# Kernel optimization log

Hardware: AMD Instinct MI355X
Metric: run time of the kernel (lower is better)

The kernel has to match this reference:

```python
import jax, jax.numpy as jnp
import numpy as np

B, L, D, H = 4, 2048, 1024, 16
DK = D // H
SCALE = 1.0 / (DK ** 0.5)


def setup_inputs() -> dict:
    key = jax.random.key(0)
    ks = jax.random.split(key, 7)
    std = 1.0 / np.sqrt(D)
    return {
        "q": jax.random.normal(ks[0], (B, L, D), jnp.float32),
        "k": jax.random.normal(ks[1], (B, L, D), jnp.float32),
        "v": jax.random.normal(ks[2], (B, L, D), jnp.float32),
        # torch nn.Linear weights: shape (out_features, in_features)
        "w_q": jax.random.normal(ks[3], (D, D), jnp.float32) * std,
        "w_k": jax.random.normal(ks[4], (D, D), jnp.float32) * std,
        "w_v": jax.random.normal(ks[5], (D, D), jnp.float32) * std,
        "w_o": jax.random.normal(ks[6], (D, D), jnp.float32) * std,
    }


def _split_heads(x):
    # (B, L, D) -> (B, H, L, DK)
    return x.reshape(B, L, H, DK).transpose(0, 2, 1, 3)


def reference(q, k, v, w_q, w_k, w_v, w_o):
    # Linear projections (no bias): y = x @ W^T
    qh = _split_heads(jnp.einsum('bld,ed->ble', q, w_q))
    kh = _split_heads(jnp.einsum('bld,ed->ble', k, w_k))
    vh = _split_heads(jnp.einsum('bld,ed->ble', v, w_v))
    # scaled dot-product attention; score is (B, H, L, L)
    score = jnp.einsum('bhqd,bhkd->bhqk', qh, kh) * SCALE
    probs = jax.nn.softmax(score, axis=-1)  # dropout p=0.0 -> identity
    attn = jnp.einsum('bhqk,bhkd->bhqd', probs, vh)
    # merge heads and output projection
    o = attn.transpose(0, 2, 1, 3).reshape(B, L, D)
    return jnp.einsum('bld,ed->ble', o, w_o)
```

## Files before the change

### kernel.cpp

```cpp
#include <hip/hip_runtime.h>
#include <stdint.h>

typedef unsigned short u16;
typedef __attribute__((ext_vector_type(8))) short short8;
typedef __attribute__((ext_vector_type(4))) float floatx4;

#define DEV __device__ __forceinline__

DEV u16 f2bf(float f) {
  union { float f; unsigned u; } x; x.f = f;
  unsigned u = x.u + 0x7fffu + ((x.u >> 16) & 1u);
  return (u16)(u >> 16);
}
DEV float scrub(float x) {
  return fminf(fmaxf(x, -65504.0f), 65504.0f);
}
DEV void async16(const void* g, void* l) {
  auto gp = reinterpret_cast<const __attribute__((address_space(1))) unsigned int*>(
      reinterpret_cast<uintptr_t>(g));
  auto lp = reinterpret_cast<__attribute__((address_space(3))) unsigned int*>(
      reinterpret_cast<uintptr_t>(l));
  __builtin_amdgcn_global_load_lds(gp, lp, 16, 0, 0);
}
DEV unsigned asu(float f) { union { float f; unsigned u; } x; x.f = f; return x.u; }
DEV float asf(unsigned u) { union { unsigned u; float f; } x; x.u = u; return x.f; }

__global__ void cvt7(const float* __restrict__ a, const float* __restrict__ b,
                     const float* __restrict__ c, const float* __restrict__ w0,
                     const float* __restrict__ w1, const float* __restrict__ w2,
                     const float* __restrict__ w3,
                     u16* __restrict__ oa, u16* __restrict__ ob, u16* __restrict__ oc,
                     u16* __restrict__ o0, u16* __restrict__ o1, u16* __restrict__ o2,
                     u16* __restrict__ o3) {
  constexpr int N4A = 1 << 21;
  constexpr int N4W = 1 << 18;
  int i4 = blockIdx.x * 256 + threadIdx.x;
  const float* s;
  u16* d;
  int off;
  if (i4 < 3 * N4A) {
    int z = i4 >> 21;
    off = i4 & (N4A - 1);
    s = z == 0 ? a : (z == 1 ? b : c);
    d = z == 0 ? oa : (z == 1 ? ob : oc);
  } else {
    int j = i4 - 3 * N4A;
    int z = j >> 18;
    off = j & (N4W - 1);
    s = z == 0 ? w0 : (z == 1 ? w1 : (z == 2 ? w2 : w3));
    d = z == 0 ? o0 : (z == 1 ? o1 : (z == 2 ? o2 : o3));
  }
  float4 v = ((const float4*)s)[off];
  union { u16 h[4]; uint2 u; } o;
  o.h[0] = f2bf(v.x); o.h[1] = f2bf(v.y); o.h[2] = f2bf(v.z); o.h[3] = f2bf(v.w);
  ((uint2*)d)[off] = o.u;
}

__global__ __launch_bounds__(256, 4) void proj3(
    const u16* __restrict__ Xq, const u16* __restrict__ Xk, const u16* __restrict__ Xv,
    const u16* __restrict__ Wq, const u16* __restrict__ Wk, const u16* __restrict__ Wv,
    u16* __restrict__ Oq, u16* __restrict__ Ok, u16* __restrict__ Ov)
{
  constexpr int K = 1024;
  constexpr float SC2 = 0.125f * 1.44269504088896f;
  int flat = blockIdx.x + 8 * (blockIdx.y + 64 * blockIdx.z);
  int swz = (flat & 7) * 192 + (flat >> 3);
  const int bx = swz & 7, by = (swz >> 3) & 63, z = swz >> 9;

  const u16* X = z == 0 ? Xq : (z == 1 ? Xk : Xv);
  const u16* W = z == 0 ? Wq : (z == 1 ? Wk : Wv);
  u16* Out = z == 0 ? Oq : (z == 1 ? Ok : Ov);

  const u16* A = (z < 2) ? W : X;
  const u16* Bp = (z < 2) ? X : W;
  const int m0 = (z < 2) ? bx * 128 : by * 128;
  const int n0 = (z < 2) ? by * 128 : bx * 128;

  const int tid = threadIdx.x;
  const int w = tid >> 6, lane = tid & 63;
  const int quad = lane >> 4, l16 = lane & 15;
  const int wm = (w & 1) * 64, wn = (w >> 1) * 64;

  __shared__ u16 As[128 * 64];
  __shared__ u16 Bs[128 * 64];

  floatx4 acc[4][4];
#pragma unroll
  for (int i = 0; i < 4; ++i)
#pragma unroll
    for (int j = 0; j < 4; ++j) acc[i][j] = (floatx4)0.0f;

  for (int k0 = 0; k0 < K; k0 += 64) {
#pragma unroll
    for (int i = 0; i < 4; ++i) {
      int lin = i * 256 + tid;
      int r = lin >> 3, sp = lin & 7, s = sp ^ (r & 7);
      async16(A + (size_t)(m0 + r) * K + k0 + s * 8, &As[lin * 8]);
    }
#pragma unroll
    for (int i = 0; i < 4; ++i) {
      int lin = i * 256 + tid;
      int r = lin >> 3, sp = lin & 7, s = sp ^ (r & 7);
      async16(Bp + (size_t)(n0 + r) * K + k0 + s * 8, &Bs[lin * 8]);
    }
    asm volatile("s_waitcnt vmcnt(0)" ::: "memory");
    __syncthreads();

#pragma unroll
    for (int kk = 0; kk < 2; ++kk) {
      short8 af[4], bf[4];
#pragma unroll
      for (int mi = 0; mi < 4; ++mi) {
        int r = wm + mi * 16 + l16;
        af[mi] = *(const short8*)&As[r * 64 + (((kk * 4 + quad) ^ (r & 7)) * 8)];
      }
#pragma unroll
      for (int ni = 0; ni < 4; ++ni) {
        int r = wn + ni * 16 + l16;
        bf[ni] = *(const short8*)&Bs[r * 64 + (((kk * 4 + quad) ^ (r & 7)) * 8)];
      }
#pragma unroll
      for (int mi = 0; mi < 4; ++mi)
#pragma unroll
        for (int ni = 0; ni < 4; ++ni)
          acc[mi][ni] = __builtin_amdgcn_mfma_f32_16x16x32_bf16(af[mi], bf[ni], acc[mi][ni], 0, 0, 0);
    }
    __syncthreads();
  }

  const float sc = (z == 0) ? SC2 : 1.0f;
#pragma unroll
  for (int mi = 0; mi < 4; ++mi) {
#pragma unroll
    for (int ni = 0; ni < 4; ++ni) {
      int rr = m0 + wm + mi * 16 + quad * 4;
      int cc = n0 + wn + ni * 16 + l16;
      u16 h0 = f2bf(sc * acc[mi][ni][0]);
      u16 h1 = f2bf(sc * acc[mi][ni][1]);
      u16 h2 = f2bf(sc * acc[mi][ni][2]);
      u16 h3 = f2bf(sc * acc[mi][ni][3]);
      uint2 dw; dw.x = h0 | ((unsigned)h1 << 16); dw.y = h2 | ((unsigned)h3 << 16);
      if (z < 2) {
        int bb = cc >> 11, ll = cc & 2047;
        int hh = rr >> 6, dk0 = rr & 63;
        *(uint2*)&Out[(((size_t)bb * 16 + hh) * 2048 + ll) * 64 + dk0] = dw;
      } else {
        int bb = rr >> 11, ll0 = rr & 2047;
        int hh = cc >> 6, dk = cc & 63;
        *(uint2*)&Out[(((size_t)bb * 16 + hh) * 64 + dk) * 2048 + ll0] = dw;
      }
    }
  }
}

__global__ __launch_bounds__(256, 2) void gemm_out(
    const u16* __restrict__ Ah, const u16* __restrict__ Wo, float* __restrict__ Out)
{
  constexpr int K = 1024;
  const int tid = threadIdx.x;
  const int w = tid >> 6, lane = tid & 63;
  const int quad = lane >> 4, l16 = lane & 15;
  int flat = blockIdx.x + 8 * blockIdx.y;
  int swz = (flat & 7) * 64 + (flat >> 3);
  const int bx = swz & 7, by = swz >> 3;
  const int m0 = by * 128, n0 = bx * 128;
  const int wm = (w & 1) * 64, wn = (w >> 1) * 64;

  __shared__ u16 SM[32768];

  auto stage = [&](int p, int k0) {
#pragma unroll
    for (int i = 0; i < 4; ++i) {
      int lin = i * 256 + tid;
      int r = lin >> 3, sp = lin & 7, s = sp ^ (r & 7);
      int row = m0 + r;
      const u16* ga = Ah + (((size_t)(row >> 11) * 16 + (k0 >> 6)) * 2048 + (row & 2047)) * 64 + s * 8;
      async16(ga, &SM[p * 8192 + lin * 8]);
    }
#pragma unroll
    for (int i = 0; i < 4; ++i) {
      int lin = i * 256 + tid;
      int r = lin >> 3, sp = lin & 7, s = sp ^ (r & 7);
      async16(Wo + (size_t)(n0 + r) * K + k0 + s * 8, &SM[16384 + p * 8192 + lin * 8]);
    }
  };

  floatx4 acc[4][4];
#pragma unroll
  for (int i = 0; i < 4; ++i)
#pragma unroll
    for (int j = 0; j < 4; ++j) acc[i][j] = (floatx4)0.0f;

  stage(0, 0);
  asm volatile("s_waitcnt vmcnt(0)" ::: "memory");
  __syncthreads();

  for (int k0 = 0; k0 < K; k0 += 64) {
    const int p = (k0 >> 6) & 1;
    if (k0 + 64 < K) stage(p ^ 1, k0 + 64);
    const u16* Asp = &SM[p * 8192];
    const u16* Bsp = &SM[16384 + p * 8192];

    __builtin_amdgcn_s_setprio(1);
#pragma unroll
    for (int kk = 0; kk < 2; ++kk) {
      short8 af[4], bf[4];
#pragma unroll
      for (int mi = 0; mi < 4; ++mi) {
        int r = wm + mi * 16 + l16;
        af[mi] = *(const short8*)&Asp[r * 64 + (((kk * 4 + quad) ^ (r & 7)) * 8)];
      }
#pragma unroll
      for (int ni = 0; ni < 4; ++ni) {
        int r = wn + ni * 16 + l16;
        bf[ni] = *(const short8*)&Bsp[r * 64 + (((kk * 4 + quad) ^ (r & 7)) * 8)];
      }
#pragma unroll
      for (int mi = 0; mi < 4; ++mi)
#pragma unroll
        for (int ni = 0; ni < 4; ++ni)
          acc[mi][ni] = __builtin_amdgcn_mfma_f32_16x16x32_bf16(af[mi], bf[ni], acc[mi][ni], 0, 0, 0);
    }
    __builtin_amdgcn_s_setprio(0);

    asm volatile("s_waitcnt vmcnt(0)" ::: "memory");
    __syncthreads();
  }

#pragma unroll
  for (int mi = 0; mi < 4; ++mi)
#pragma unroll
    for (int ni = 0; ni < 4; ++ni) {
      int rr = m0 + wm + mi * 16 + quad * 4;
      int cc = n0 + wn + ni * 16 + l16;
#pragma unroll
      for (int reg = 0; reg < 4; ++reg)
        Out[(size_t)(rr + reg) * 1024 + cc] = scrub(acc[mi][ni][reg]);
    }
}

__global__ __launch_bounds__(256, 4) void attn3(
    const u16* Qh, const u16* __restrict__ Kh,
    const u16* __restrict__ VT, u16* O)
{
  constexpr int L = 2048, DK = 64, H = 16;
  const int tid = threadIdx.x;
  const int w = tid >> 6, lane = tid & 63;
  const int quad = lane >> 4, l16 = lane & 15;
  int flat = blockIdx.x + 16 * (blockIdx.y + 16 * blockIdx.z);
  int swz = (flat & 7) * 128 + (flat >> 3);
  const int q0 = (swz & 15) * 128;
  const int bh = swz >> 4;

  __shared__ u16 SM[4 * 64 * 64];
  u16* const QP = &SM[8192];
  char* const SMb = (char*)&SM[0];

  const u16* Qg = Qh + ((size_t)bh * L + q0) * DK;
  const u16* Kb = Kh + (size_t)bh * L * DK;
  const u16* Vb = VT + (size_t)bh * DK * L;

#pragma unroll
  for (int i = 0; i < 4; ++i) {
    int lin = i * 256 + tid;
    int r = lin >> 3, sp = lin & 7, s = sp ^ (r & 7);
    async16(Qg + (size_t)r * DK + s * 8, &QP[lin * 8]);
  }

  const int rA = tid >> 3;
  const int sA = (tid & 7) ^ (rA & 7);
  const u16* kg0 = Kb + (size_t)rA * DK + sA * 8;
  const u16* kg1 = kg0 + 32 * DK;
  const u16* vg0 = Vb + (size_t)rA * L + sA * 8;
  const u16* vg1 = vg0 + (size_t)32 * L;
  u16* const ldsB0 = &SM[tid * 8];
  u16* const ldsB1 = &SM[8192 + tid * 8];

  async16(kg0, ldsB0);
  async16(kg1, ldsB0 + 2048);
  async16(vg0, ldsB0 + 4096);
  async16(vg1, ldsB0 + 6144);
  kg0 += 64 * DK; kg1 += 64 * DK; vg0 += 64; vg1 += 64;

  asm volatile("s_waitcnt vmcnt(0)" ::: "memory");
  __syncthreads();

  short8 qf[2][2];
#pragma unroll
  for (int mi = 0; mi < 2; ++mi)
#pragma unroll
    for (int kk = 0; kk < 2; ++kk) {
      int r = w * 32 + mi * 16 + l16;
      qf[mi][kk] = *(const short8*)&QP[r * 64 + (((kk * 4 + quad) ^ (r & 7)) * 8)];
    }
  asm volatile("s_waitcnt lgkmcnt(0)" ::: "memory");
  __syncthreads();

  const int l7 = l16 & 7, qh2 = quad >> 1, qo = (quad & 1) * 8;
  int ka[2], vo[4];
#pragma unroll
  for (int kk = 0; kk < 2; ++kk)
    ka[kk] = l16 * 128 + (((kk * 4 + quad) ^ l7) * 16);
#pragma unroll
  for (int j = 0; j < 4; ++j)
    vo[j] = l16 * 128 + (((qh2 + 2 * j) ^ l7) * 16) + qo;

  short8 onesv;
#pragma unroll
  for (int j = 0; j < 8; ++j) onesv[j] = (short)0x3F80;

  floatx4 oT[4][2];
  floatx4 lacc[2];
#pragma unroll
  for (int nd = 0; nd < 4; ++nd)
#pragma unroll
    for (int mi = 0; mi < 2; ++mi) oT[nd][mi] = (floatx4)0.0f;
  lacc[0] = (floatx4)0.0f;
  lacc[1] = (floatx4)0.0f;

  auto body = [&](int PB, u16* ldsN, bool more) {
    if (more) {
      async16(kg0, ldsN);
      async16(kg1, ldsN + 2048);
      async16(vg0, ldsN + 4096);
      async16(vg1, ldsN + 6144);
      kg0 += 64 * DK; kg1 += 64 * DK; vg0 += 64; vg1 += 64;
    }

    floatx4 sT[4][2];
#pragma unroll
    for (int t = 0; t < 4; ++t)
#pragma unroll
      for (int mi = 0; mi < 2; ++mi) sT[t][mi] = (floatx4)0.0f;
    __builtin_amdgcn_s_setprio(1);
#pragma unroll
    for (int kk = 0; kk < 2; ++kk)
#pragma unroll
      for (int t = 0; t < 4; ++t) {
        short8 kf = *(const short8*)(SMb + PB + t * 2048 + ka[kk]);
#pragma unroll
        for (int mi = 0; mi < 2; ++mi)
          sT[t][mi] = __builtin_amdgcn_mfma_f32_16x16x32_bf16(kf, qf[mi][kk], sT[t][mi], 0, 0, 0);
      }
    __builtin_amdgcn_s_setprio(0);

#pragma unroll
    for (int t = 0; t < 4; ++t)
#pragma unroll
      for (int mi = 0; mi < 2; ++mi)
#pragma unroll
        for (int r = 0; r < 4; ++r) sT[t][mi][r] = __builtin_amdgcn_exp2f(sT[t][mi][r]);

    short8 pf[2][2];
#pragma unroll
    for (int g = 0; g < 2; ++g)
#pragma unroll
      for (int mi = 0; mi < 2; ++mi) {
        union { unsigned u[4]; short8 v; } up;
        up.u[0] = __builtin_amdgcn_perm(asu(sT[2 * g][mi][1]), asu(sT[2 * g][mi][0]), 0x07060302u);
        up.u[1] = __builtin_amdgcn_perm(asu(sT[2 * g][mi][3]), asu(sT[2 * g][mi][2]), 0x07060302u);
        up.u[2] = __builtin_amdgcn_perm(asu(sT[2 * g + 1][mi][1]), asu(sT[2 * g + 1][mi][0]), 0x07060302u);
        up.u[3] = __builtin_amdgcn_perm(asu(sT[2 * g + 1][mi][3]), asu(sT[2 * g + 1][mi][2]), 0x07060302u);
        pf[g][mi] = up.v;
      }

    __builtin_amdgcn_s_setprio(1);
#pragma unroll
    for (int g = 0; g < 2; ++g) {
#pragma unroll
      for (int nd = 0; nd < 4; ++nd) {
        union { uint2 ab[2]; short8 v; } uv;
        uv.ab[0] = *(const uint2*)(SMb + PB + 8192 + nd * 2048 + vo[2 * g]);
        uv.ab[1] = *(const uint2*)(SMb + PB + 8192 + nd * 2048 + vo[2 * g + 1]);
#pragma unroll
        for (int mi = 0; mi < 2; ++mi)
          oT[nd][mi] = __builtin_amdgcn_mfma_f32_16x16x32_bf16(uv.v, pf[g][mi], oT[nd][mi], 0, 0, 0);
      }
#pragma unroll
      for (int mi = 0; mi < 2; ++mi)
        lacc[mi] = __builtin_amdgcn_mfma_f32_16x16x32_bf16(onesv, pf[g][mi], lacc[mi], 0, 0, 0);
    }
    __builtin_amdgcn_s_setprio(0);

    asm volatile("s_waitcnt vmcnt(0)" ::: "memory");
    __syncthreads();
  };

  for (int j0 = 0; j0 < L; j0 += 128) {
    asm volatile("" : "+v"(ka[0]), "+v"(ka[1]),
                      "+v"(vo[0]), "+v"(vo[1]), "+v"(vo[2]), "+v"(vo[3]));
    body(0, ldsB1, true);
    body(16384, ldsB0, j0 + 128 < L);
  }

#pragma unroll
  for (int mi = 0; mi < 2; ++mi) {
    float inv = 1.0f / fmaxf(lacc[mi][0], 1e-30f);
    int token = q0 + w * 32 + mi * 16 + l16;
#pragma unroll
    for (int nd = 0; nd < 4; ++nd) {
      u16 h0 = f2bf(scrub(oT[nd][mi][0] * inv));
      u16 h1 = f2bf(scrub(oT[nd][mi][1] * inv));
      u16 h2 = f2bf(scrub(oT[nd][mi][2] * inv));
      u16 h3 = f2bf(scrub(oT[nd][mi][3] * inv));
      uint2 dw; dw.x = h0 | ((unsigned)h1 << 16); dw.y = h2 | ((unsigned)h3 << 16);
      *(uint2*)&O[((size_t)bh * L + token) * 64 + nd * 16 + quad * 4] = dw;
    }
  }
}

extern "C" void kernel_launch(void* const* d_in, const int* in_sizes, int n_in,
                              void* d_out, int out_size, void* d_ws, size_t ws_size,
                              hipStream_t stream) {
  const float* q  = (const float*)d_in[0];
  const float* k  = (const float*)d_in[1];
  const float* v  = (const float*)d_in[2];
  const float* wq = (const float*)d_in[3];
  const float* wk = (const float*)d_in[4];
  const float* wv = (const float*)d_in[5];
  const float* wo = (const float*)d_in[6];
  float* out = (float*)d_out;

  const size_t NE = (size_t)4 * 16 * 2048 * 64;
  const size_t WN = (size_t)1024 * 1024;

  u16* qb  = (u16*)d_ws;
  u16* kb  = qb + NE;
  u16* vb  = kb + NE;
  u16* wqb = vb + NE;
  u16* wkb = wqb + WN;
  u16* wvb = wkb + WN;
  u16* wob = wvb + WN;
  u16* Qh  = wob + WN;
  u16* Kh  = (u16*)d_out;
  u16* VTg = Kh + NE;

  cvt7<<<dim3(28672), 256, 0, stream>>>(
      q, k, v, wq, wk, wv, wo, qb, kb, vb, wqb, wkb, wvb, wob);

  dim3 g1(8, 64, 3);
  proj3<<<g1, dim3(256), 0, stream>>>(qb, kb, vb, wqb, wkb, wvb, Qh, Kh, VTg);

  dim3 g2(16, 16, 4);
  attn3<<<g2, dim3(256), 0, stream>>>(Qh, Kh, VTg, Qh);

  dim3 g3(8, 64, 1);
  gemm_out<<<g3, dim3(256), 0, stream>>>(Qh, wob, out);
}
```

Measured before the change: 305.5 us.

## Fuse fp32-to-bf16 conversion of inputs and weights into projection GEMM staging

```diff
diff --git a/kernel.cpp b/kernel.cpp
--- a/kernel.cpp
+++ b/kernel.cpp
@@ -24,41 +24,23 @@
 }
 DEV unsigned asu(float f) { union { float f; unsigned u; } x; x.f = f; return x.u; }
 DEV float asf(unsigned u) { union { unsigned u; float f; } x; x.u = u; return x.f; }
-
-__global__ void cvt7(const float* __restrict__ a, const float* __restrict__ b,
-                     const float* __restrict__ c, const float* __restrict__ w0,
-                     const float* __restrict__ w1, const float* __restrict__ w2,
-                     const float* __restrict__ w3,
-                     u16* __restrict__ oa, u16* __restrict__ ob, u16* __restrict__ oc,
-                     u16* __restrict__ o0, u16* __restrict__ o1, u16* __restrict__ o2,
-                     u16* __restrict__ o3) {
-  constexpr int N4A = 1 << 21;
-  constexpr int N4W = 1 << 18;
-  int i4 = blockIdx.x * 256 + threadIdx.x;
-  const float* s;
-  u16* d;
-  int off;
-  if (i4 < 3 * N4A) {
-    int z = i4 >> 21;
-    off = i4 & (N4A - 1);
-    s = z == 0 ? a : (z == 1 ? b : c);
-    d = z == 0 ? oa : (z == 1 ? ob : oc);
-  } else {
-    int j = i4 - 3 * N4A;
-    int z = j >> 18;
-    off = j & (N4W - 1);
-    s = z == 0 ? w0 : (z == 1 ? w1 : (z == 2 ? w2 : w3));
-    d = z == 0 ? o0 : (z == 1 ? o1 : (z == 2 ? o2 : o3));
-  }
-  float4 v = ((const float4*)s)[off];
+DEV unsigned cvtpk(float lo, float hi) {
+  unsigned r;
+  asm("v_cvt_pk_bf16_f32 %0, %1, %2" : "=v"(r) : "v"(lo), "v"(hi));
+  return r;
+}
+
+__global__ void cvt1(const float* __restrict__ s, u16* __restrict__ d) {
+  int i = blockIdx.x * 256 + threadIdx.x;
+  float4 v = ((const float4*)s)[i];
   union { u16 h[4]; uint2 u; } o;
   o.h[0] = f2bf(v.x); o.h[1] = f2bf(v.y); o.h[2] = f2bf(v.z); o.h[3] = f2bf(v.w);
-  ((uint2*)d)[off] = o.u;
-}
-
-__global__ __launch_bounds__(256, 4) void proj3(
-    const u16* __restrict__ Xq, const u16* __restrict__ Xk, const u16* __restrict__ Xv,
-    const u16* __restrict__ Wq, const u16* __restrict__ Wk, const u16* __restrict__ Wv,
+  ((uint2*)d)[i] = o.u;
+}
+
+__global__ __launch_bounds__(256, 3) void proj3(
+    const float* __restrict__ Xq, const float* __restrict__ Xk, const float* __restrict__ Xv,
+    const float* __restrict__ Wq, const float* __restrict__ Wk, const float* __restrict__ Wv,
     u16* __restrict__ Oq, u16* __restrict__ Ok, u16* __restrict__ Ov)
 {
   constexpr int K = 1024;
@@ -67,12 +49,12 @@
   int swz = (flat & 7) * 192 + (flat >> 3);
   const int bx = swz & 7, by = (swz >> 3) & 63, z = swz >> 9;
 
-  const u16* X = z == 0 ? Xq : (z == 1 ? Xk : Xv);
-  const u16* W = z == 0 ? Wq : (z == 1 ? Wk : Wv);
+  const float* X = z == 0 ? Xq : (z == 1 ? Xk : Xv);
+  const float* W = z == 0 ? Wq : (z == 1 ? Wk : Wv);
   u16* Out = z == 0 ? Oq : (z == 1 ? Ok : Ov);
 
-  const u16* A = (z < 2) ? W : X;
-  const u16* Bp = (z < 2) ? X : W;
+  const float* A = (z < 2) ? W : X;
+  const float* Bp = (z < 2) ? X : W;
   const int m0 = (z < 2) ? bx * 128 : by * 128;
   const int n0 = (z < 2) ? by * 128 : bx * 128;
 
@@ -84,26 +66,34 @@
   __shared__ u16 As[128 * 64];
   __shared__ u16 Bs[128 * 64];
 
-  floatx4 acc[4][4];
-#pragma unroll
-  for (int i = 0; i < 4; ++i)
-#pragma unroll
-    for (int j = 0; j < 4; ++j) acc[i][j] = (floatx4)0.0f;
-
-  for (int k0 = 0; k0 < K; k0 += 64) {
+  const int rS = tid >> 3, spS = tid & 7;
+  const int sS = spS ^ (rS & 7);
+
+  auto stageF = [&](const float* src, int row0, u16* dst, int k0) {
 #pragma unroll
     for (int i = 0; i < 4; ++i) {
       int lin = i * 256 + tid;
-      int r = lin >> 3, sp = lin & 7, s = sp ^ (r & 7);
-      async16(A + (size_t)(m0 + r) * K + k0 + s * 8, &As[lin * 8]);
-    }
-#pragma unroll
-    for (int i = 0; i < 4; ++i) {
-      int lin = i * 256 + tid;
-      int r = lin >> 3, sp = lin & 7, s = sp ^ (r & 7);
-      async16(Bp + (size_t)(n0 + r) * K + k0 + s * 8, &Bs[lin * 8]);
-    }
-    asm volatile("s_waitcnt vmcnt(0)" ::: "memory");
+      const float* g = src + (size_t)(row0 + rS + i * 32) * K + k0 + sS * 8;
+      float4 u0 = *(const float4*)g;
+      float4 u1 = *(const float4*)(g + 4);
+      union { unsigned u[4]; uint4 q; } pk;
+      pk.u[0] = cvtpk(u0.x, u0.y);
+      pk.u[1] = cvtpk(u0.z, u0.w);
+      pk.u[2] = cvtpk(u1.x, u1.y);
+      pk.u[3] = cvtpk(u1.z, u1.w);
+      *(uint4*)&dst[lin * 8] = pk.q;
+    }
+  };
+
+  floatx4 acc[4][4];
+#pragma unroll
+  for (int i = 0; i < 4; ++i)
+#pragma unroll
+    for (int j = 0; j < 4; ++j) acc[i][j] = (floatx4)0.0f;
+
+  for (int k0 = 0; k0 < K; k0 += 64) {
+    stageF(A, m0, As, k0);
+    stageF(Bp, n0, Bs, k0);
     __syncthreads();
 
 #pragma unroll
@@ -424,22 +414,15 @@
   const size_t NE = (size_t)4 * 16 * 2048 * 64;
   const size_t WN = (size_t)1024 * 1024;
 
-  u16* qb  = (u16*)d_ws;
-  u16* kb  = qb + NE;
-  u16* vb  = kb + NE;
-  u16* wqb = vb + NE;
-  u16* wkb = wqb + WN;
-  u16* wvb = wkb + WN;
-  u16* wob = wvb + WN;
+  u16* wob = (u16*)d_ws;
   u16* Qh  = wob + WN;
   u16* Kh  = (u16*)d_out;
   u16* VTg = Kh + NE;
 
-  cvt7<<<dim3(28672), 256, 0, stream>>>(
-      q, k, v, wq, wk, wv, wo, qb, kb, vb, wqb, wkb, wvb, wob);
+  cvt1<<<dim3(1024), 256, 0, stream>>>(wo, wob);
 
   dim3 g1(8, 64, 3);
-  proj3<<<g1, dim3(256), 0, stream>>>(qb, kb, vb, wqb, wkb, wvb, Qh, Kh, VTg);
+  proj3<<<g1, dim3(256), 0, stream>>>(q, k, v, wq, wk, wv, Qh, Kh, VTg);
 
   dim3 g2(16, 16, 4);
   attn3<<<g2, dim3(256), 0, stream>>>(Qh, Kh, VTg, Qh);
```

New measurement: 402.8 us. 1.32x slower.
